# Kernel tuning notes

Measured on AMD Instinct MI355X. Metric: run time of the kernel, lower is better.

Reference implementation:

```python
import jax, jax.numpy as jnp
import numpy as np

EMB = 512
HEADS = 8
HEAD_DIM = EMB // HEADS
FFN = 2048
RECENCY = 0.05
NEG = -1e9


def setup_inputs() -> dict:
    key = jax.random.key(0)
    ks = jax.random.split(key, 16)
    s = 0.02
    d = {
        'x': jax.random.normal(ks[0], (2, 2048, EMB), jnp.float32),
        'wq': jax.random.normal(ks[1], (EMB, EMB), jnp.float32) * s,
        'bq': jnp.zeros((EMB,), jnp.float32),
        'wk': jax.random.normal(ks[2], (EMB, EMB), jnp.float32) * s,
        'bk': jnp.zeros((EMB,), jnp.float32),
        'wv': jax.random.normal(ks[3], (EMB, EMB), jnp.float32) * s,
        'bv': jnp.zeros((EMB,), jnp.float32),
        'wo': jax.random.normal(ks[4], (EMB, EMB), jnp.float32) * s,
        'bo': jnp.zeros((EMB,), jnp.float32),
        'ln1_g': jnp.ones((EMB,), jnp.float32),
        'ln1_b': jnp.zeros((EMB,), jnp.float32),
        'w1': jax.random.normal(ks[5], (EMB, FFN), jnp.float32) * s,
        'b1': jnp.zeros((FFN,), jnp.float32),
        'w2': jax.random.normal(ks[6], (FFN, EMB), jnp.float32) * s,
        'b2': jnp.zeros((EMB,), jnp.float32),
        'ln2_g': jnp.ones((EMB,), jnp.float32),
        'ln2_b': jnp.zeros((EMB,), jnp.float32),
    }
    return d


def _layernorm(x, g, b, eps=1e-5):
    mu = jnp.mean(x, axis=-1, keepdims=True)
    var = jnp.var(x, axis=-1, keepdims=True)
    return (x - mu) * jax.lax.rsqrt(var + eps) * g + b


def _split_heads(x):
    b, s, _ = x.shape
    return x.reshape(b, s, HEADS, HEAD_DIM).transpose(0, 2, 1, 3)  # [b,h,s,d]


def _block(x, wq, bq, wk, bk, wv, bv, wo, bo, ln1_g, ln1_b, w1, b1, w2, b2, ln2_g, ln2_b):
    b, s, _ = x.shape
    q = _split_heads(x @ wq + bq)
    k = _split_heads(x @ wk + bk)
    v = _split_heads(x @ wv + bv)
    scores = jnp.einsum('bhqd,bhkd->bhqk', q, k) / np.sqrt(HEAD_DIM)
    pos = jnp.arange(s)
    dist = jnp.abs(pos[:, None] - pos[None, :]).astype(scores.dtype)
    bias = -RECENCY * dist  # recency (ALiBi-like) bias
    bias = jnp.where(pos[None, :] > pos[:, None], NEG, bias)  # causal
    scores = scores + bias[None, None]
    attn = jax.nn.softmax(scores, axis=-1)
    ctx = jnp.einsum('bhqk,bhkd->bhqd', attn, v)
    ctx = ctx.transpose(0, 2, 1, 3).reshape(b, s, EMB)
    attn_out = ctx @ wo + bo
    x = _layernorm(x + attn_out, ln1_g, ln1_b)
    ffn = jax.nn.relu(x @ w1 + b1) @ w2 + b2
    x = _layernorm(x + ffn, ln2_g, ln2_b)
    return x


def reference(x, wq, bq, wk, bk, wv, bv, wo, bo, ln1_g, ln1_b, w1, b1, w2, b2, ln2_g, ln2_b):
    return _block(x, wq, bq, wk, bk, wv, bv, wo, bo, ln1_g, ln1_b, w1, b1, w2, b2, ln2_g, ln2_b)
```

## Files before the change

kernel.cpp:

```cpp
#include <hip/hip_runtime.h>
#include <hip/hip_bf16.h>
#include <stdint.h>

using u16 = unsigned short;
using bf16x8 = __attribute__((ext_vector_type(8))) short;
using f32x4  = __attribute__((ext_vector_type(4))) float;

__device__ __forceinline__ u16 f2bf(float f) {
    union { float f; unsigned u; } c; c.f = f;
    unsigned u = c.u;
    return (u16)((u + 0x7fffu + ((u >> 16) & 1u)) >> 16);
}
__device__ __forceinline__ float bf2f(u16 h) {
    union { unsigned u; float f; } c; c.u = ((unsigned)h) << 16;
    return c.f;
}

#define EMB 512
#define SEQ 2048
#define BATCH 2
#define NTOK (BATCH * SEQ)
#define FFN_DIM 2048
#define NEGINF (-1e9f)
#define LOG2E 1.44269504f

__global__ void conv_all(const float* __restrict__ x,
                         const float* __restrict__ wq, const float* __restrict__ wk,
                         const float* __restrict__ wv, const float* __restrict__ bq,
                         const float* __restrict__ bk, const float* __restrict__ bv,
                         const float* __restrict__ wo, const float* __restrict__ w1,
                         const float* __restrict__ w2,
                         u16* __restrict__ xb, u16* __restrict__ wqkv_t,
                         float* __restrict__ bqkv, u16* __restrict__ wo_t,
                         u16* __restrict__ w1_t, u16* __restrict__ w2_t) {
    int i = blockIdx.x * 256 + threadIdx.x;
    if (i < 2097152) {
        xb[i] = f2bf(x[i]);
    } else if (i < 2883584) {
        int idx = i - 2097152;
        int n = idx >> 9, k = idx & 511;
        int sel = n >> 9, nn = n & 511;
        const float* w = (sel == 0) ? wq : (sel == 1) ? wk : wv;
        wqkv_t[idx] = f2bf(w[k * 512 + nn]);
        if (k == 0) {
            const float* b = (sel == 0) ? bq : (sel == 1) ? bk : bv;
            bqkv[n] = b[nn];
        }
    } else if (i < 3145728) {
        int idx = i - 2883584;
        int n = idx >> 9, k = idx & 511;
        wo_t[idx] = f2bf(wo[k * 512 + n]);
    } else if (i < 4194304) {
        int idx = i - 3145728;
        int n = idx >> 9, k = idx & 511;
        w1_t[idx] = f2bf(w1[k * 2048 + n]);
    } else if (i < 5242880) {
        int idx = i - 4194304;
        int n = idx >> 11, k = idx & 2047;
        w2_t[idx] = f2bf(w2[k * 512 + n]);
    }
}

template <int EPI, int BM, int BN>
__global__ __launch_bounds__(256) void gemm_bt(
    const u16* __restrict__ A, const u16* __restrict__ Bt,
    const float* __restrict__ bias, const float* __restrict__ res,
    u16* __restrict__ outb, float* __restrict__ outf, u16* __restrict__ vt_out,
    int M, int N, int K) {
    constexpr int RM = BM / 32, RN = BN / 32 > 0 ? BN / 32 : 1;
    __shared__ __align__(16) u16 a_s[BM * 72];
    __shared__ __align__(16) u16 b_s[BN * 72];
    const int t = threadIdx.x;
    const int wave = t >> 6, lane = t & 63;
    const int wr = wave >> 1, wc = wave & 1;
    const int lr = lane & 15, lh = lane >> 4;
    const int m0 = blockIdx.x * BM, n0 = blockIdx.y * BN;

    f32x4 acc[RM][RN] = {};

    for (int kt = 0; kt < K; kt += 64) {
        __syncthreads();
#pragma unroll
        for (int i = 0; i < BM / 32; ++i) {
            int chunk = t + 256 * i;
            int row = chunk >> 3, c8 = (chunk & 7) * 8;
            *(int4*)&a_s[row * 72 + c8] = *(const int4*)&A[(size_t)(m0 + row) * K + kt + c8];
        }
#pragma unroll
        for (int i = 0; i < (BN + 31) / 32; ++i) {
            int chunk = t + 256 * i;
            int row = chunk >> 3, c8 = (chunk & 7) * 8;
            if (BN >= 32 || chunk < BN * 8)
                *(int4*)&b_s[row * 72 + c8] = *(const int4*)&Bt[(size_t)(n0 + row) * K + kt + c8];
        }
        __syncthreads();
#pragma unroll
        for (int ks = 0; ks < 64; ks += 32) {
            bf16x8 af[RM], bfr[RN];
#pragma unroll
            for (int m = 0; m < RM; ++m)
                af[m] = *(const bf16x8*)&a_s[(wr * (BM / 2) + m * 16 + lr) * 72 + ks + lh * 8];
#pragma unroll
            for (int n = 0; n < RN; ++n)
                bfr[n] = *(const bf16x8*)&b_s[(wc * (BN / 2) + n * 16 + lr) * 72 + ks + lh * 8];
#pragma unroll
            for (int m = 0; m < RM; ++m)
#pragma unroll
                for (int n = 0; n < RN; ++n)
                    acc[m][n] = __builtin_amdgcn_mfma_f32_16x16x32_bf16(af[m], bfr[n], acc[m][n], 0, 0, 0);
        }
    }

#pragma unroll
    for (int m = 0; m < RM; ++m) {
        int row = m0 + wr * (BM / 2) + m * 16 + lh * 4;
#pragma unroll
        for (int n = 0; n < RN; ++n) {
            int col = n0 + wc * (BN / 2) + n * 16 + lr;
            float bv = bias[col];
            if (EPI == 3 && col >= 1024) {
                int dg = col - 1024, hh = dg >> 6, dd = dg & 63;
                int bb = row >> 11, ss = row & 2047;
                ushort4 pk;
                pk.x = f2bf(acc[m][n][0] + bv);
                pk.y = f2bf(acc[m][n][1] + bv);
                pk.z = f2bf(acc[m][n][2] + bv);
                pk.w = f2bf(acc[m][n][3] + bv);
                *(ushort4*)&vt_out[((size_t)((bb * 8 + hh) * 64 + dd)) * SEQ + ss] = pk;
            } else {
#pragma unroll
                for (int r = 0; r < 4; ++r) {
                    float v = acc[m][n][r] + bv;
                    size_t o = (size_t)(row + r) * N + col;
                    if (EPI == 1) outb[o] = f2bf(v > 0.f ? v : 0.f);
                    else if (EPI == 2) outf[o] = v + res[o];
                    else outb[o] = f2bf(v);
                }
            }
        }
    }
}

__global__ __launch_bounds__(256) void attn_part(
    const u16* __restrict__ qkv, const u16* __restrict__ vt,
    u16* __restrict__ opart, float* __restrict__ lpart) {
    const int bid = blockIdx.x;
    const int xcd = bid & 7, jj = bid >> 3;
    const int bh = 2 * xcd + (jj & 1);
    const int b = bh >> 3, h = bh & 7;
    const int w = threadIdx.x >> 6, lane = threadIdx.x & 63;
    const int lr = lane & 15, lh = lane >> 4;
    __shared__ __align__(16) u16 p_all[4][16 * 72];
    u16* p_lds = p_all[w];

    const int f = (jj >> 1) * 4 + w;
    const int c = (f >= 560) ? 7 : (f >= 528) ? 6 : (f >= 480) ? 5 : (f >= 416) ? 4
                : (f >= 336) ? 3 : (f >= 240) ? 2 : (f >= 128) ? 1 : 0;
    const int qt = 16 * c + (f - (136 * c - 8 * c * c));
    const int q0 = qt * 16;
    const int nt = (qt >> 2) + 1;
    const int kend = (4 * c + 4 < nt) ? (4 * c + 4) : nt;

    const size_t qbase = (size_t)(b * SEQ + q0 + lr) * 1536 + h * 64;
    bf16x8 aq0 = *(const bf16x8*)&qkv[qbase + lh * 8];
    bf16x8 aq1 = *(const bf16x8*)&qkv[qbase + 32 + lh * 8];

    const float SC = 0.125f * LOG2E;
    const float RC = 0.05f * LOG2E;

    f32x4 acc_o[4] = {};
    float tsum[4] = {0.f, 0.f, 0.f, 0.f};

    for (int kt = 4 * c; kt < kend; ++kt) {
        f32x4 s[4];
#pragma unroll
        for (int n = 0; n < 4; ++n) {
            int kcol = kt * 64 + n * 16 + lr;
            size_t kbase = (size_t)(b * SEQ + kcol) * 1536 + 512 + h * 64;
            bf16x8 bk0 = *(const bf16x8*)&qkv[kbase + lh * 8];
            bf16x8 bk1 = *(const bf16x8*)&qkv[kbase + 32 + lh * 8];
            f32x4 z = {};
            z = __builtin_amdgcn_mfma_f32_16x16x32_bf16(aq0, bk0, z, 0, 0, 0);
            s[n] = __builtin_amdgcn_mfma_f32_16x16x32_bf16(aq1, bk1, z, 0, 0, 0);
        }
#pragma unroll
        for (int n = 0; n < 4; ++n) {
            int k = kt * 64 + n * 16 + lr;
#pragma unroll
            for (int r = 0; r < 4; ++r) {
                int q = q0 + lh * 4 + r;
                float v = s[n][r] * SC + ((k > q) ? NEGINF : -RC * (float)(q - k));
                float p = exp2f(v);
                tsum[r] += p;
                p_lds[(lh * 4 + r) * 72 + n * 16 + lr] = f2bf(p);
            }
        }
#pragma unroll
        for (int ks = 0; ks < 2; ++ks) {
            bf16x8 pa = *(const bf16x8*)&p_lds[lr * 72 + ks * 32 + lh * 8];
#pragma unroll
            for (int nd = 0; nd < 4; ++nd) {
                size_t vrow = (size_t)(bh * 64 + nd * 16 + lr) * SEQ + kt * 64 + ks * 32 + lh * 8;
                bf16x8 bv = *(const bf16x8*)&vt[vrow];
                acc_o[nd] = __builtin_amdgcn_mfma_f32_16x16x32_bf16(pa, bv, acc_o[nd], 0, 0, 0);
            }
        }
    }

#pragma unroll
    for (int msk = 1; msk < 16; msk <<= 1)
#pragma unroll
        for (int r = 0; r < 4; ++r) tsum[r] += __shfl_xor(tsum[r], msk);

    const int idx = bh * 576 + f;
    u16* ob = opart + (size_t)idx * 1024;
#pragma unroll
    for (int nd = 0; nd < 4; ++nd) {
        ushort4 pk;
        pk.x = f2bf(acc_o[nd][0]); pk.y = f2bf(acc_o[nd][1]);
        pk.z = f2bf(acc_o[nd][2]); pk.w = f2bf(acc_o[nd][3]);
        *(ushort4*)&ob[(nd * 16 + lr) * 16 + lh * 4] = pk;
    }
    if (lr == 0) {
#pragma unroll
        for (int r = 0; r < 4; ++r)
            lpart[idx * 16 + lh * 4 + r] = tsum[r];
    }
}

__global__ __launch_bounds__(256) void attn_merge(
    const u16* __restrict__ opart, const float* __restrict__ lpart, u16* __restrict__ ctx) {
    const int bid = blockIdx.x;
    const int xcd = bid & 7, j = bid >> 3;
    const int bh = 2 * xcd + (j & 1);
    const int qt = j >> 1;
    const int b = bh >> 3, h = bh & 7;
    const int t = threadIdx.x;
    const int nt = (qt >> 2) + 1;
    const int nc = (nt + 3) >> 2;
#pragma unroll
    for (int i = 0; i < 4; ++i) {
        int e = t + 256 * i;
        int row = e >> 6, col = e & 63;
        float num = 0.f, den = 0.f;
        for (int c = 0; c < nc; ++c) {
            int idx = bh * 576 + (136 * c - 8 * c * c) + (qt - 16 * c);
            num += bf2f(opart[(size_t)idx * 1024 + col * 16 + row]);
            den += lpart[idx * 16 + row];
        }
        ctx[(size_t)(b * SEQ + qt * 16 + row) * EMB + h * 64 + col] = f2bf(num / den);
    }
}

template <bool WRITE_BF>
__global__ __launch_bounds__(256) void lnorm(
    const float* __restrict__ in, const float* __restrict__ g, const float* __restrict__ bta,
    float* __restrict__ outf, u16* __restrict__ outb) {
    const int row = blockIdx.x * 4 + (threadIdx.x >> 6);
    const int lane = threadIdx.x & 63;
    const float* p = in + (size_t)row * EMB;
    float4 v0 = ((const float4*)p)[lane];
    float4 v1 = ((const float4*)p)[64 + lane];
    float sum = v0.x + v0.y + v0.z + v0.w + v1.x + v1.y + v1.z + v1.w;
    float sq = v0.x*v0.x + v0.y*v0.y + v0.z*v0.z + v0.w*v0.w
             + v1.x*v1.x + v1.y*v1.y + v1.z*v1.z + v1.w*v1.w;
#pragma unroll
    for (int msk = 1; msk < 64; msk <<= 1) {
        sum += __shfl_xor(sum, msk);
        sq  += __shfl_xor(sq, msk);
    }
    float mu = sum * (1.f / EMB);
    float var = sq * (1.f / EMB) - mu * mu;
    float rs = rsqrtf(var + 1e-5f);
    float4 g0 = ((const float4*)g)[lane], g1 = ((const float4*)g)[64 + lane];
    float4 b0 = ((const float4*)bta)[lane], b1 = ((const float4*)bta)[64 + lane];
    float o0x = (v0.x - mu) * rs * g0.x + b0.x;
    float o0y = (v0.y - mu) * rs * g0.y + b0.y;
    float o0z = (v0.z - mu) * rs * g0.z + b0.z;
    float o0w = (v0.w - mu) * rs * g0.w + b0.w;
    float o1x = (v1.x - mu) * rs * g1.x + b1.x;
    float o1y = (v1.y - mu) * rs * g1.y + b1.y;
    float o1z = (v1.z - mu) * rs * g1.z + b1.z;
    float o1w = (v1.w - mu) * rs * g1.w + b1.w;
    float4* po = (float4*)(outf + (size_t)row * EMB);
    po[lane] = make_float4(o0x, o0y, o0z, o0w);
    po[64 + lane] = make_float4(o1x, o1y, o1z, o1w);
    if (WRITE_BF) {
        u16* pb = outb + (size_t)row * EMB;
        int c = lane * 4;
        pb[c] = f2bf(o0x); pb[c + 1] = f2bf(o0y); pb[c + 2] = f2bf(o0z); pb[c + 3] = f2bf(o0w);
        pb[256 + c] = f2bf(o1x); pb[256 + c + 1] = f2bf(o1y);
        pb[256 + c + 2] = f2bf(o1z); pb[256 + c + 3] = f2bf(o1w);
    }
}

extern "C" void kernel_launch(void* const* d_in, const int* in_sizes, int n_in,
                              void* d_out, int out_size, void* d_ws, size_t ws_size,
                              hipStream_t stream) {
    const float* x     = (const float*)d_in[0];
    const float* wq    = (const float*)d_in[1];
    const float* bq    = (const float*)d_in[2];
    const float* wk    = (const float*)d_in[3];
    const float* bk    = (const float*)d_in[4];
    const float* wv    = (const float*)d_in[5];
    const float* bv    = (const float*)d_in[6];
    const float* wo    = (const float*)d_in[7];
    const float* bo    = (const float*)d_in[8];
    const float* ln1_g = (const float*)d_in[9];
    const float* ln1_b = (const float*)d_in[10];
    const float* w1    = (const float*)d_in[11];
    const float* b1    = (const float*)d_in[12];
    const float* w2    = (const float*)d_in[13];
    const float* b2    = (const float*)d_in[14];
    const float* ln2_g = (const float*)d_in[15];
    const float* ln2_b = (const float*)d_in[16];
    float* out = (float*)d_out;

    char* w = (char*)d_ws;
    size_t off = 0;
    auto nxt = [&](size_t bytes) -> void* {
        void* p = w + off;
        off = (off + bytes + 255) & ~(size_t)255;
        return p;
    };
    u16*   xb      = (u16*)nxt((size_t)NTOK * EMB * 2);
    u16*   wqkv_t  = (u16*)nxt((size_t)1536 * 512 * 2);
    float* bqkv    = (float*)nxt(1536 * 4);
    u16*   wo_t    = (u16*)nxt((size_t)512 * 512 * 2);
    u16*   w1_t    = (u16*)nxt((size_t)2048 * 512 * 2);
    u16*   w2_t    = (u16*)nxt((size_t)512 * 2048 * 2);
    u16*   qkvb    = (u16*)nxt((size_t)NTOK * 1536 * 2);
    u16*   vt      = (u16*)nxt((size_t)16 * 64 * SEQ * 2);
    u16*   ctxb    = (u16*)nxt((size_t)NTOK * EMB * 2);
    float* ybuf    = (float*)nxt((size_t)NTOK * EMB * 4);
    float* x1      = (float*)nxt((size_t)NTOK * EMB * 4);
    u16*   x1b     = (u16*)nxt((size_t)NTOK * EMB * 2);
    u16*   hb      = (u16*)nxt((size_t)NTOK * FFN_DIM * 2);

    u16*   opart = (u16*)ybuf;
    float* lpart = (float*)((char*)ybuf + 18874368);

    conv_all<<<20480, 256, 0, stream>>>(x, wq, wk, wv, bq, bk, bv, wo, w1, w2,
                                        xb, wqkv_t, bqkv, wo_t, w1_t, w2_t);

    gemm_bt<3, 64, 64><<<dim3(64, 24), 256, 0, stream>>>(
        xb, wqkv_t, bqkv, nullptr, qkvb, nullptr, vt, NTOK, 1536, 512);
    attn_part<<<2304, 256, 0, stream>>>(qkvb, vt, opart, lpart);
    attn_merge<<<2048, 256, 0, stream>>>(opart, lpart, ctxb);
    gemm_bt<2, 64, 32><<<dim3(64, 16), 256, 0, stream>>>(
        ctxb, wo_t, bo, x, nullptr, ybuf, nullptr, NTOK, 512, 512);
    lnorm<true><<<NTOK / 4, 256, 0, stream>>>(ybuf, ln1_g, ln1_b, x1, x1b);
    gemm_bt<1, 64, 64><<<dim3(64, 32), 256, 0, stream>>>(
        x1b, w1_t, b1, nullptr, hb, nullptr, nullptr, NTOK, FFN_DIM, 512);
    gemm_bt<2, 64, 32><<<dim3(64, 16), 256, 0, stream>>>(
        hb, w2_t, b2, x1, nullptr, ybuf, nullptr, NTOK, EMB, FFN_DIM);
    lnorm<false><<<NTOK / 4, 256, 0, stream>>>(ybuf, ln2_g, ln2_b, out, nullptr);
}
```

Measured before the change: 292.5 us.

## Split each query tile's key range across four waves with fixed-stride partials

Each block now handles one query tile, longest first, and splits its causal key-tile range evenly over its four waves. Before, each wave owned a fixed chunk of up to four key tiles taken from a flattened triangular index. The causal mask is applied only on the diagonal key tile, so the other tiles skip the compare and select. Partials always come in four chunks, so the merge kernel stages them through LDS with coalesced loads and sums a fixed four terms. Tiles near the start of the sequence leave some waves with little or no work, and empty chunks still write zero partials.

New measurement: 270.1 us. 7.7% less time.

```diff
diff --git a/kernel.cpp b/kernel.cpp
--- a/kernel.cpp
+++ b/kernel.cpp
@@ -145,21 +145,20 @@
     const u16* __restrict__ qkv, const u16* __restrict__ vt,
     u16* __restrict__ opart, float* __restrict__ lpart) {
     const int bid = blockIdx.x;
-    const int xcd = bid & 7, jj = bid >> 3;
-    const int bh = 2 * xcd + (jj & 1);
+    const int xcd = bid & 7, j = bid >> 3;
+    const int bh = 2 * xcd + (j & 1);
+    const int qt = 127 - (j >> 1);
     const int b = bh >> 3, h = bh & 7;
     const int w = threadIdx.x >> 6, lane = threadIdx.x & 63;
     const int lr = lane & 15, lh = lane >> 4;
     __shared__ __align__(16) u16 p_all[4][16 * 72];
     u16* p_lds = p_all[w];
 
-    const int f = (jj >> 1) * 4 + w;
-    const int c = (f >= 560) ? 7 : (f >= 528) ? 6 : (f >= 480) ? 5 : (f >= 416) ? 4
-                : (f >= 336) ? 3 : (f >= 240) ? 2 : (f >= 128) ? 1 : 0;
-    const int qt = 16 * c + (f - (136 * c - 8 * c * c));
     const int q0 = qt * 16;
-    const int nt = (qt >> 2) + 1;
-    const int kend = (4 * c + 4 < nt) ? (4 * c + 4) : nt;
+    const int nt = (q0 + 15) / 64 + 1;
+    const int clen = (nt + 3) >> 2;
+    const int k0 = w * clen;
+    const int k1 = (k0 + clen < nt) ? (k0 + clen) : nt;
 
     const size_t qbase = (size_t)(b * SEQ + q0 + lr) * 1536 + h * 64;
     bf16x8 aq0 = *(const bf16x8*)&qkv[qbase + lh * 8];
@@ -171,7 +170,7 @@
     f32x4 acc_o[4] = {};
     float tsum[4] = {0.f, 0.f, 0.f, 0.f};
 
-    for (int kt = 4 * c; kt < kend; ++kt) {
+    for (int kt = k0; kt < k1; ++kt) {
         f32x4 s[4];
 #pragma unroll
         for (int n = 0; n < 4; ++n) {
@@ -183,16 +182,30 @@
             z = __builtin_amdgcn_mfma_f32_16x16x32_bf16(aq0, bk0, z, 0, 0, 0);
             s[n] = __builtin_amdgcn_mfma_f32_16x16x32_bf16(aq1, bk1, z, 0, 0, 0);
         }
-#pragma unroll
-        for (int n = 0; n < 4; ++n) {
-            int k = kt * 64 + n * 16 + lr;
-#pragma unroll
-            for (int r = 0; r < 4; ++r) {
-                int q = q0 + lh * 4 + r;
-                float v = s[n][r] * SC + ((k > q) ? NEGINF : -RC * (float)(q - k));
-                float p = exp2f(v);
-                tsum[r] += p;
-                p_lds[(lh * 4 + r) * 72 + n * 16 + lr] = f2bf(p);
+        if (kt == nt - 1) {
+#pragma unroll
+            for (int n = 0; n < 4; ++n) {
+                int k = kt * 64 + n * 16 + lr;
+#pragma unroll
+                for (int r = 0; r < 4; ++r) {
+                    int q = q0 + lh * 4 + r;
+                    float v = s[n][r] * SC + ((k > q) ? NEGINF : -RC * (float)(q - k));
+                    float p = exp2f(v);
+                    tsum[r] += p;
+                    p_lds[(lh * 4 + r) * 72 + n * 16 + lr] = f2bf(p);
+                }
+            }
+        } else {
+#pragma unroll
+            for (int n = 0; n < 4; ++n) {
+                int k = kt * 64 + n * 16 + lr;
+#pragma unroll
+                for (int r = 0; r < 4; ++r) {
+                    int q = q0 + lh * 4 + r;
+                    float p = exp2f(s[n][r] * SC - RC * (float)(q - k));
+                    tsum[r] += p;
+                    p_lds[(lh * 4 + r) * 72 + n * 16 + lr] = f2bf(p);
+                }
             }
         }
 #pragma unroll
@@ -212,7 +225,7 @@
 #pragma unroll
         for (int r = 0; r < 4; ++r) tsum[r] += __shfl_xor(tsum[r], msk);
 
-    const int idx = bh * 576 + f;
+    const int idx = (w * 128 + qt) * 16 + bh;
     u16* ob = opart + (size_t)idx * 1024;
 #pragma unroll
     for (int nd = 0; nd < 4; ++nd) {
@@ -235,19 +248,27 @@
     const int bh = 2 * xcd + (j & 1);
     const int qt = j >> 1;
     const int b = bh >> 3, h = bh & 7;
+    __shared__ __align__(16) u16 o_lds[4][1024];
+    __shared__ float l_lds[64];
     const int t = threadIdx.x;
-    const int nt = (qt >> 2) + 1;
-    const int nc = (nt + 3) >> 2;
+#pragma unroll
+    for (int c = 0; c < 4; ++c) {
+        const int idx = (c * 128 + qt) * 16 + bh;
+        ((ushort4*)o_lds[c])[t] = ((const ushort4*)(opart + (size_t)idx * 1024))[t];
+    }
+    if (t < 64) {
+        int c = t >> 4, row = t & 15;
+        int idx = (c * 128 + qt) * 16 + bh;
+        l_lds[t] = lpart[idx * 16 + row];
+    }
+    __syncthreads();
 #pragma unroll
     for (int i = 0; i < 4; ++i) {
         int e = t + 256 * i;
         int row = e >> 6, col = e & 63;
-        float num = 0.f, den = 0.f;
-        for (int c = 0; c < nc; ++c) {
-            int idx = bh * 576 + (136 * c - 8 * c * c) + (qt - 16 * c);
-            num += bf2f(opart[(size_t)idx * 1024 + col * 16 + row]);
-            den += lpart[idx * 16 + row];
-        }
+        float den = l_lds[row] + l_lds[16 + row] + l_lds[32 + row] + l_lds[48 + row];
+        float num = bf2f(o_lds[0][col * 16 + row]) + bf2f(o_lds[1][col * 16 + row])
+                  + bf2f(o_lds[2][col * 16 + row]) + bf2f(o_lds[3][col * 16 + row]);
         ctx[(size_t)(b * SEQ + qt * 16 + row) * EMB + h * 64 + col] = f2bf(num / den);
     }
 }
@@ -338,14 +359,14 @@
     u16*   hb      = (u16*)nxt((size_t)NTOK * FFN_DIM * 2);
 
     u16*   opart = (u16*)ybuf;
-    float* lpart = (float*)((char*)ybuf + 18874368);
+    float* lpart = (float*)((char*)ybuf + 16777216);
 
     conv_all<<<20480, 256, 0, stream>>>(x, wq, wk, wv, bq, bk, bv, wo, w1, w2,
                                         xb, wqkv_t, bqkv, wo_t, w1_t, w2_t);
 
     gemm_bt<3, 64, 64><<<dim3(64, 24), 256, 0, stream>>>(
         xb, wqkv_t, bqkv, nullptr, qkvb, nullptr, vt, NTOK, 1536, 512);
-    attn_part<<<2304, 256, 0, stream>>>(qkvb, vt, opart, lpart);
+    attn_part<<<2048, 256, 0, stream>>>(qkvb, vt, opart, lpart);
     attn_merge<<<2048, 256, 0, stream>>>(opart, lpart, ctxb);
     gemm_bt<2, 64, 32><<<dim3(64, 16), 256, 0, stream>>>(
         ctxb, wo_t, bo, x, nullptr, ybuf, nullptr, NTOK, 512, 512);
```
